# Performance work log

Hardware: AMD Instinct MI355X
Metric: run time of the kernel (lower is better)

The kernel has to match this reference:

```python
import jax, jax.numpy as jnp
import numpy as np

MARGIN = 0.3
LOSS_FLOOR = 1e-06


def setup_inputs() -> dict:
    key = jax.random.key(0)
    k1, k2 = jax.random.split(key)
    embeddings = jax.random.normal(k1, (8192, 128), dtype=jnp.float32)
    labels = jax.random.randint(k2, (8192,), 0, 512, dtype=jnp.int64)
    return {"embeddings": embeddings, "labels": labels}


def _pairwise_dist(x):
    # Euclidean cdist via the GEMM identity; clamp for numerical safety.
    sq = jnp.sum(x * x, axis=1)  # [N]
    d2 = sq[:, None] + sq[None, :] - 2.0 * (x @ x.T)  # [N, N]
    return jnp.sqrt(jnp.maximum(d2, 1e-12))


def reference(embeddings, labels):
    dist = _pairwise_dist(embeddings)  # [N, N]
    same = labels[None, :] == labels[:, None]  # [N, N]
    n = embeddings.shape[0]
    eye = jnp.eye(n, dtype=bool)
    mask_pos = same & ~eye
    mask_neg = ~same  # diagonal is same-label, so already excluded

    neg_inf = jnp.float32(-jnp.inf)
    pos_inf = jnp.float32(jnp.inf)
    hardest_pos = jnp.max(jnp.where(mask_pos, dist, neg_inf), axis=1)  # [N]
    hardest_neg = jnp.min(jnp.where(mask_neg, dist, pos_inf), axis=1)  # [N]

    valid = jnp.any(mask_pos, axis=1) & jnp.any(mask_neg, axis=1)  # [N]
    per_row = jnp.maximum(hardest_pos - hardest_neg + MARGIN, LOSS_FLOOR)
    num_valid = jnp.sum(valid)
    total = jnp.sum(jnp.where(valid, per_row, 0.0))
    return jnp.where(num_valid > 0, total / jnp.maximum(num_valid, 1), 0.0).astype(embeddings.dtype)
```

## Files before the change

### kernel.cpp

```cpp
#include <hip/hip_runtime.h>
#include <math.h>


#define NROWS 8192
#define DIM   128
#define NLAB  512
#define JSPLIT 32
#define JCHUNK (NROWS / JSPLIT)
#define NSUB   4
#define SUBROWS 64

typedef short bf16x8 __attribute__((ext_vector_type(8)));
typedef float f32x4  __attribute__((ext_vector_type(4)));

static __device__ __forceinline__ unsigned short f2bf(float f) {
    unsigned u = __float_as_uint(f);
    unsigned r = (u + 0x7FFFu + ((u >> 16) & 1u)) >> 16;
    return (unsigned short)r;
}

static __device__ __forceinline__ void gload_lds16(const void* g, void* l) {
    __builtin_amdgcn_global_load_lds(
        (const __attribute__((address_space(1))) unsigned int*)g,
        (__attribute__((address_space(3))) unsigned int*)l, 16, 0, 0);
}

__global__ __launch_bounds__(512) void histscan_kernel(
    const int* __restrict__ labels, int* __restrict__ hist,
    int* __restrict__ base, int* __restrict__ cursor,
    float* __restrict__ gsum, float* __restrict__ gcnt,
    unsigned* __restrict__ done) {
    __shared__ int h[NLAB];
    __shared__ int wpre[8];
    int t = threadIdx.x;
    h[t] = 0;
    __syncthreads();
    const int4* l4 = (const int4*)labels;
#pragma unroll
    for (int i = 0; i < NROWS / 4 / 512; ++i) {
        int4 L = l4[i * 512 + t];
        atomicAdd(&h[L.x], 1); atomicAdd(&h[L.y], 1);
        atomicAdd(&h[L.z], 1); atomicAdd(&h[L.w], 1);
    }
    __syncthreads();
    int v = h[t];
    int sc = v;
#pragma unroll
    for (int d = 1; d < 64; d <<= 1) {
        int y = __shfl_up(sc, d, 64);
        if ((t & 63) >= d) sc += y;
    }
    if ((t & 63) == 63) wpre[t >> 6] = sc;
    __syncthreads();
    if (t < 8) {
        int w = wpre[t];
        int p = w;
#pragma unroll
        for (int d = 1; d < 8; d <<= 1) {
            int y = __shfl_up(p, d, 64);
            if (t >= d) p += y;
        }
        wpre[t] = p - w;
    }
    __syncthreads();
    int incl = sc + wpre[t >> 6];
    int b = incl - v;
    hist[t] = v;
    base[t] = b;
    cursor[t] = b;
    if (t == 0) { *gsum = 0.f; *gcnt = 0.f; *done = 0u; }
}

__global__ __launch_bounds__(256) void scatter_kernel(
    const float* __restrict__ x, const int* __restrict__ labels,
    const int* __restrict__ base, const int* __restrict__ hist,
    int* __restrict__ cursor, float* __restrict__ sqp,
    float* __restrict__ sqh, int* __restrict__ labp,
    int2* __restrict__ rng, unsigned short* __restrict__ xb) {
    int t = blockIdx.x * 256 + threadIdx.x;
    int row = t >> 5;
    int c = t & 31;
    int wl = threadIdx.x & 63;
    float4 v = ((const float4*)x)[t];
    float ps = v.x * v.x + v.y * v.y + v.z * v.z + v.w * v.w;
#pragma unroll
    for (int sft = 1; sft < 32; sft <<= 1) ps += __shfl_xor(ps, sft, 64);
    int p;
    if (c == 0) {
        int l = labels[row];
        p = atomicAdd(&cursor[l], 1);
        sqp[p] = ps;
        sqh[p] = -0.5f * ps;
        labp[p] = l;
        rng[p] = make_int2(base[l], base[l] + hist[l]);
    }
    p = __shfl(p, wl & 32, 64);
    ushort4 ob;
    ob.x = f2bf(v.x); ob.y = f2bf(v.y); ob.z = f2bf(v.z); ob.w = f2bf(v.w);
    ((ushort4*)xb)[p * 32 + c] = ob;
}

__global__ __launch_bounds__(256, 4) void pair_kernel(
    const unsigned short* __restrict__ xb, const float* __restrict__ sqh,
    const int* __restrict__ labp, const int2* __restrict__ rng,
    float* __restrict__ hpp, float* __restrict__ hnp) {
    __shared__ __attribute__((aligned(16))) unsigned char abuf[2][SUBROWS * 256];
    __shared__ __attribute__((aligned(16))) float sqs[JCHUNK];

    const int tid = threadIdx.x;
    const int lane = tid & 63;
    const int wid = tid >> 6;
    const int q = lane >> 4;
    const int r = lane & 15;
    const int ibase = blockIdx.x * 256 + wid * 64;
    const int jbase = blockIdx.y * JCHUNK;

    sqs[tid] = sqh[jbase + tid];

    bf16x8 bfrag[4][4];
    int labi[4];
    unsigned ovm[4];
#pragma unroll
    for (int sub = 0; sub < 4; ++sub) {
        int irow = ibase + sub * 16 + r;
        labi[sub] = labp[irow];
        int2 g = rng[irow];
        int a = g.x - jbase;
        int b = g.y - jbase;
        int ttmin = a >> 4;
        if (ttmin < 0) ttmin = 0;
        if (ttmin > 16) ttmin = 16;
        int ttmax = (b - 1) >> 4;
        if (ttmax > 15) ttmax = 15;
        ovm[sub] = (ttmax >= ttmin) ? ((2u << ttmax) - (1u << ttmin)) : 0u;
#pragma unroll
        for (int ks = 0; ks < 4; ++ks)
            bfrag[sub][ks] = *(const bf16x8*)(xb + (size_t)irow * DIM + ks * 32 + q * 8);
    }
    const unsigned ovu = ovm[0] | ovm[1] | ovm[2] | ovm[3];

    float hp[4] = {INFINITY, INFINITY, INFINITY, INFINITY};
    float hn[4] = {-INFINITY, -INFINITY, -INFINITY, -INFINITY};

    auto stage = [&](int s, int buf) {
        const char* gb = (const char*)xb + (size_t)(jbase + s * SUBROWS) * 256;
        unsigned char* lb = &abuf[buf][0];
#pragma unroll
        for (int p = 0; p < 4; ++p) {
            int row = wid * 16 + p * 4 + (lane >> 4);
            int colb = (lane & 15) * 16;
            const void* g = gb + row * 256 + (colb ^ ((row & 15) << 4));
            void* l = lb + wid * 4096 + p * 1024;
            gload_lds16(g, l);
        }
    };

    auto compute_tile = [&](int s, int buf, int t) {
        const unsigned char* lb = &abuf[buf][0];
        const int tt = s * 4 + t;
        bf16x8 af[4];
        const int rowb = (t * 16 + r) * 256;
        const int sw = r << 4;
#pragma unroll
        for (int ks = 0; ks < 4; ++ks)
            af[ks] = *(const bf16x8*)(lb + rowb + ((ks * 64 + q * 16) ^ sw));
        f32x4 ci = *(const f32x4*)(&sqs[s * SUBROWS + t * 16 + q * 4]);

        if (!__any((int)((ovu >> tt) & 1u))) {
#pragma unroll
            for (int sub = 0; sub < 4; ++sub) {
                f32x4 acc = ci;
                acc = __builtin_amdgcn_mfma_f32_16x16x32_bf16(af[0], bfrag[sub][0], acc, 0, 0, 0);
                acc = __builtin_amdgcn_mfma_f32_16x16x32_bf16(af[1], bfrag[sub][1], acc, 0, 0, 0);
                acc = __builtin_amdgcn_mfma_f32_16x16x32_bf16(af[2], bfrag[sub][2], acc, 0, 0, 0);
                acc = __builtin_amdgcn_mfma_f32_16x16x32_bf16(af[3], bfrag[sub][3], acc, 0, 0, 0);
                hn[sub] = fmaxf(hn[sub],
                                fmaxf(fmaxf(acc[0], acc[1]), fmaxf(acc[2], acc[3])));
            }
        } else {
            const int j0 = jbase + tt * 16;
            int4 labj = *(const int4*)(labp + j0 + q * 4);
#pragma unroll
            for (int sub = 0; sub < 4; ++sub) {
                f32x4 acc = ci;
                acc = __builtin_amdgcn_mfma_f32_16x16x32_bf16(af[0], bfrag[sub][0], acc, 0, 0, 0);
                acc = __builtin_amdgcn_mfma_f32_16x16x32_bf16(af[1], bfrag[sub][1], acc, 0, 0, 0);
                acc = __builtin_amdgcn_mfma_f32_16x16x32_bf16(af[2], bfrag[sub][2], acc, 0, 0, 0);
                acc = __builtin_amdgcn_mfma_f32_16x16x32_bf16(af[3], bfrag[sub][3], acc, 0, 0, 0);
                if (__any((int)((ovm[sub] >> tt) & 1u))) {
                    const int li = labi[sub];
                    float u0 = acc[0], u1 = acc[1], u2 = acc[2], u3 = acc[3];
                    hp[sub] = fminf(hp[sub], (labj.x == li) ? u0 : INFINITY);
                    hn[sub] = fmaxf(hn[sub], (labj.x == li) ? -INFINITY : u0);
                    hp[sub] = fminf(hp[sub], (labj.y == li) ? u1 : INFINITY);
                    hn[sub] = fmaxf(hn[sub], (labj.y == li) ? -INFINITY : u1);
                    hp[sub] = fminf(hp[sub], (labj.z == li) ? u2 : INFINITY);
                    hn[sub] = fmaxf(hn[sub], (labj.z == li) ? -INFINITY : u2);
                    hp[sub] = fminf(hp[sub], (labj.w == li) ? u3 : INFINITY);
                    hn[sub] = fmaxf(hn[sub], (labj.w == li) ? -INFINITY : u3);
                } else {
                    hn[sub] = fmaxf(hn[sub],
                                    fmaxf(fmaxf(acc[0], acc[1]), fmaxf(acc[2], acc[3])));
                }
            }
        }
    };

    stage(0, 0);
    __syncthreads();
#pragma unroll
    for (int s = 0; s < NSUB; ++s) {
        if (s + 1 < NSUB) stage(s + 1, (s + 1) & 1);
#pragma unroll
        for (int t = 0; t < 4; ++t) compute_tile(s, s & 1, t);
        __syncthreads();
    }

#pragma unroll
    for (int sub = 0; sub < 4; ++sub) {
        hp[sub] = fminf(hp[sub], __shfl_xor(hp[sub], 16, 64));
        hp[sub] = fminf(hp[sub], __shfl_xor(hp[sub], 32, 64));
        hn[sub] = fmaxf(hn[sub], __shfl_xor(hn[sub], 16, 64));
        hn[sub] = fmaxf(hn[sub], __shfl_xor(hn[sub], 32, 64));
    }
    if (lane < 16) {
        const int pbase = blockIdx.y * NROWS;
#pragma unroll
        for (int sub = 0; sub < 4; ++sub) {
            int irow = ibase + sub * 16 + lane;
            hpp[pbase + irow] = hp[sub];
            hnp[pbase + irow] = hn[sub];
        }
    }
}

__global__ __launch_bounds__(256) void reduce_kernel(
    const float* __restrict__ hpp, const float* __restrict__ hnp,
    const float* __restrict__ sqp, const int* __restrict__ labp,
    const int* __restrict__ hist, float* __restrict__ gsum,
    float* __restrict__ gcnt, unsigned* __restrict__ done,
    float* __restrict__ out) {
    int row = blockIdx.x * 256 + threadIdx.x;
    float mnp = INFINITY, mxn = -INFINITY;
#pragma unroll 8
    for (int p = 0; p < JSPLIT; ++p) {
        mnp = fminf(mnp, hpp[p * NROWS + row]);
        mxn = fmaxf(mxn, hnp[p * NROWS + row]);
    }
    float s = sqp[row];
    int h = hist[labp[row]];
    float sum = 0.f, cnt = 0.f;
    if (h >= 2 && h < NROWS) {
        float dp = sqrtf(fmaxf(s - 2.f * mnp, 1e-12f));
        float dn = sqrtf(fmaxf(s - 2.f * mxn, 1e-12f));
        sum = fmaxf(dp - dn + 0.3f, 1e-6f);
        cnt = 1.f;
    }
#pragma unroll
    for (int sh = 1; sh < 64; sh <<= 1) {
        sum += __shfl_xor(sum, sh, 64);
        cnt += __shfl_xor(cnt, sh, 64);
    }
    __shared__ float ss[4], sc[4];
    int w = threadIdx.x >> 6;
    if ((threadIdx.x & 63) == 0) { ss[w] = sum; sc[w] = cnt; }
    __syncthreads();
    if (threadIdx.x == 0) {
        atomicAdd(gsum, ss[0] + ss[1] + ss[2] + ss[3]);
        atomicAdd(gcnt, sc[0] + sc[1] + sc[2] + sc[3]);
        __threadfence();
        unsigned t = atomicAdd(done, 1u);
        if (t == gridDim.x - 1) {
            float S = atomicAdd(gsum, 0.f);
            float C = atomicAdd(gcnt, 0.f);
            out[0] = (C > 0.f) ? S / C : 0.f;
        }
    }
}

extern "C" void kernel_launch(void* const* d_in, const int* in_sizes, int n_in,
                              void* d_out, int out_size, void* d_ws, size_t ws_size,
                              hipStream_t stream) {
    const float* x = (const float*)d_in[0];
    const int* labels = (const int*)d_in[1];
    float* out = (float*)d_out;

    char* ws = (char*)d_ws;
    int* hist = (int*)ws;
    int* base = (int*)(ws + 2048);
    int* cursor = (int*)(ws + 4096);
    float* gsum = (float*)(ws + 6144);
    float* gcnt = (float*)(ws + 6148);
    unsigned* done = (unsigned*)(ws + 6152);
    float* sqp = (float*)(ws + 8192);
    float* sqh = (float*)(ws + 40960);
    int* labp = (int*)(ws + 73728);
    int2* rng = (int2*)(ws + 106496);
    float* hpp = (float*)(ws + 172032);
    float* hnp = (float*)(ws + 1220608);
    unsigned short* xb = (unsigned short*)(ws + 2269184);

    histscan_kernel<<<1, 512, 0, stream>>>(labels, hist, base, cursor, gsum, gcnt, done);
    scatter_kernel<<<(NROWS * 32) / 256, 256, 0, stream>>>(
        x, labels, base, hist, cursor, sqp, sqh, labp, rng, xb);
    pair_kernel<<<dim3(NROWS / 256, JSPLIT), 256, 0, stream>>>(
        xb, sqh, labp, rng, hpp, hnp);
    reduce_kernel<<<NROWS / 256, 256, 0, stream>>>(
        hpp, hnp, sqp, labp, hist, gsum, gcnt, done, out);
}
```

Measured before the change: 99.77 us.

## Deepen LDS staging pipeline to four smaller buffers with partial vmcnt waits

Splits the 256-row j-chunk into eight 32-row stages held in a four-deep LDS ring, prefetching two stages ahead. Full __syncthreads are replaced with explicit s_waitcnt vmcnt counts and a raw s_barrier, so loads for later stages stay in flight while the current one is computed. The per-row label register array is dropped and the label is reloaded from global memory inside the diagonal-tile path to reduce register pressure. This risks barrier-ordering hazards, since a single barrier per stage now guards both buffer reuse and load completion.

```diff
diff --git a/kernel.cpp b/kernel.cpp
--- a/kernel.cpp
+++ b/kernel.cpp
@@ -7,8 +7,8 @@
 #define NLAB  512
 #define JSPLIT 32
 #define JCHUNK (NROWS / JSPLIT)
-#define NSUB   4
-#define SUBROWS 64
+#define NSUBT  8
+#define SUBROWS 32
 
 typedef short bf16x8 __attribute__((ext_vector_type(8)));
 typedef float f32x4  __attribute__((ext_vector_type(4)));
@@ -104,7 +104,7 @@
     const unsigned short* __restrict__ xb, const float* __restrict__ sqh,
     const int* __restrict__ labp, const int2* __restrict__ rng,
     float* __restrict__ hpp, float* __restrict__ hnp) {
-    __shared__ __attribute__((aligned(16))) unsigned char abuf[2][SUBROWS * 256];
+    __shared__ __attribute__((aligned(16))) unsigned char abuf[4][SUBROWS * 256];
     __shared__ __attribute__((aligned(16))) float sqs[JCHUNK];
 
     const int tid = threadIdx.x;
@@ -118,12 +118,10 @@
     sqs[tid] = sqh[jbase + tid];
 
     bf16x8 bfrag[4][4];
-    int labi[4];
     unsigned ovm[4];
 #pragma unroll
     for (int sub = 0; sub < 4; ++sub) {
         int irow = ibase + sub * 16 + r;
-        labi[sub] = labp[irow];
         int2 g = rng[irow];
         int a = g.x - jbase;
         int b = g.y - jbase;
@@ -146,25 +144,25 @@
         const char* gb = (const char*)xb + (size_t)(jbase + s * SUBROWS) * 256;
         unsigned char* lb = &abuf[buf][0];
 #pragma unroll
-        for (int p = 0; p < 4; ++p) {
-            int row = wid * 16 + p * 4 + (lane >> 4);
+        for (int p = 0; p < 2; ++p) {
+            int row = wid * 8 + p * 4 + (lane >> 4);
             int colb = (lane & 15) * 16;
             const void* g = gb + row * 256 + (colb ^ ((row & 15) << 4));
-            void* l = lb + wid * 4096 + p * 1024;
+            void* l = lb + wid * 2048 + p * 1024;
             gload_lds16(g, l);
         }
     };
 
     auto compute_tile = [&](int s, int buf, int t) {
         const unsigned char* lb = &abuf[buf][0];
-        const int tt = s * 4 + t;
+        const int tt = s * 2 + t;
         bf16x8 af[4];
         const int rowb = (t * 16 + r) * 256;
         const int sw = r << 4;
 #pragma unroll
         for (int ks = 0; ks < 4; ++ks)
             af[ks] = *(const bf16x8*)(lb + rowb + ((ks * 64 + q * 16) ^ sw));
-        f32x4 ci = *(const f32x4*)(&sqs[s * SUBROWS + t * 16 + q * 4]);
+        f32x4 ci = *(const f32x4*)(&sqs[tt * 16 + q * 4]);
 
         if (!__any((int)((ovu >> tt) & 1u))) {
 #pragma unroll
@@ -188,7 +186,7 @@
                 acc = __builtin_amdgcn_mfma_f32_16x16x32_bf16(af[2], bfrag[sub][2], acc, 0, 0, 0);
                 acc = __builtin_amdgcn_mfma_f32_16x16x32_bf16(af[3], bfrag[sub][3], acc, 0, 0, 0);
                 if (__any((int)((ovm[sub] >> tt) & 1u))) {
-                    const int li = labi[sub];
+                    const int li = labp[ibase + sub * 16 + r];
                     float u0 = acc[0], u1 = acc[1], u2 = acc[2], u3 = acc[3];
                     hp[sub] = fminf(hp[sub], (labj.x == li) ? u0 : INFINITY);
                     hn[sub] = fmaxf(hn[sub], (labj.x == li) ? -INFINITY : u0);
@@ -207,14 +205,28 @@
     };
 
     stage(0, 0);
-    __syncthreads();
-#pragma unroll
-    for (int s = 0; s < NSUB; ++s) {
-        if (s + 1 < NSUB) stage(s + 1, (s + 1) & 1);
-#pragma unroll
-        for (int t = 0; t < 4; ++t) compute_tile(s, s & 1, t);
-        __syncthreads();
-    }
+    stage(1, 1);
+    __syncthreads();
+
+#define PAIR_ITER(S, VMSTR)                                              \
+    {                                                                    \
+        if ((S) + 2 < NSUBT) stage((S) + 2, ((S) + 2) & 3);              \
+        asm volatile("s_waitcnt " VMSTR ::: "memory");                   \
+        __builtin_amdgcn_s_barrier();                                    \
+        __builtin_amdgcn_sched_barrier(0);                               \
+        compute_tile((S), (S) & 3, 0);                                   \
+        compute_tile((S), (S) & 3, 1);                                   \
+    }
+
+    PAIR_ITER(0, "vmcnt(4)")
+    PAIR_ITER(1, "vmcnt(4)")
+    PAIR_ITER(2, "vmcnt(4)")
+    PAIR_ITER(3, "vmcnt(4)")
+    PAIR_ITER(4, "vmcnt(4)")
+    PAIR_ITER(5, "vmcnt(4)")
+    PAIR_ITER(6, "vmcnt(2)")
+    PAIR_ITER(7, "vmcnt(0)")
+#undef PAIR_ITER
 
 #pragma unroll
     for (int sub = 0; sub < 4; ++sub) {
```

New measurement: 103.2 us. 3.4% more time.
